# Kernel optimization log

Measured on AMD Instinct MI355X. Metric: run time of the kernel, lower is better.

Reference implementation:

```python
import jax, jax.numpy as jnp
import numpy as np

SOS_INDEX = 0


def setup_inputs() -> dict:
    key = jax.random.key(0)
    ks = jax.random.split(key, 12)
    T, B, H, V = 64, 1024, 512, 512
    s = 1.0 / np.sqrt(H)
    inp = {
        "target_var": jax.random.randint(ks[0], (T, B), 0, V, dtype=jnp.int64),
        "target_max_len": T,
        "encoder_hidden": jax.random.normal(ks[1], (B, H), jnp.float32),
        "encoder_cell": jax.random.normal(ks[2], (B, H), jnp.float32),
        "embedding": jax.random.normal(ks[3], (V, H), jnp.float32) * s,
        "W_ih": jax.random.normal(ks[4], (4 * H, H), jnp.float32) * s,
        "W_hh": jax.random.normal(ks[5], (4 * H, H), jnp.float32) * s,
        "b_ih": jax.random.normal(ks[6], (4 * H,), jnp.float32) * s,
        "b_hh": jax.random.normal(ks[7], (4 * H,), jnp.float32) * s,
        "W_out": jax.random.normal(ks[8], (V, H), jnp.float32) * s,
        "b_out": jax.random.normal(ks[9], (V,), jnp.float32) * s,
    }
    return inp


def reference(target_var, target_max_len, encoder_hidden, encoder_cell,
              embedding, W_ih, W_hh, b_ih, b_hh, W_out, b_out):
    B = target_var.shape[1]
    H = encoder_hidden.shape[1]
    # initial decoder input: embedding of SOS token for every batch element
    x0 = jnp.broadcast_to(embedding[SOS_INDEX], (B, H))
    bias = b_ih + b_hh  # [4H]

    def step(carry, _):
        x, h, c = carry
        # PyTorch LSTMCell: gate order i, f, g, o
        gates = x @ W_ih.T + h @ W_hh.T + bias  # [B, 4H]
        i, f, g, o = jnp.split(gates, 4, axis=-1)
        c_new = jax.nn.sigmoid(f) * c + jax.nn.sigmoid(i) * jnp.tanh(g)
        h_new = jax.nn.sigmoid(o) * jnp.tanh(c_new)
        logits = h_new @ W_out.T + b_out  # [B, V]
        # greedy decoding (topk(1)) -> next input embedding
        nxt = embedding[jnp.argmax(logits, axis=-1)]  # [B, H]
        return (nxt, h_new, c_new), logits

    _, outputs = jax.lax.scan(step, (x0, encoder_hidden, encoder_cell),
                              None, length=target_max_len)
    return outputs  # [T, B, V]
```

## Files before the change

kernel.cpp:

```cpp
#include <hip/hip_runtime.h>
#include <math.h>

constexpr int T_STEPS = 64;
constexpr int B_SZ = 1024;
constexpr int H_SZ = 512;
constexpr int V_SZ = 512;
constexpr int G_SZ = 4 * H_SZ;

typedef _Float16 half8 __attribute__((ext_vector_type(8)));
typedef _Float16 half4 __attribute__((ext_vector_type(4)));
typedef float f32x4 __attribute__((ext_vector_type(4)));

__device__ __forceinline__ float4 ld4(const float* p) {
    return *reinterpret_cast<const float4*>(p);
}
__device__ __forceinline__ void st4(float* p, float4 v) {
    *reinterpret_cast<float4*>(p) = v;
}
__device__ __forceinline__ float sigf(float x) { return 1.f / (1.f + expf(-x)); }

__device__ __forceinline__ unsigned long long pack_vc(float v, int col) {
    unsigned u = __float_as_uint(v);
    unsigned key = (u & 0x80000000u) ? ~u : (u | 0x80000000u);
    return ((unsigned long long)key << 32) | (unsigned)(511 - col);
}

__global__ __launch_bounds__(256) void cvt_pair(
    const float* __restrict__ x, _Float16* __restrict__ hi,
    _Float16* __restrict__ lo)
{
    const int i4 = blockIdx.x * 256 + threadIdx.x;
    const float4 v = ld4(x + (size_t)i4 * 4);
    half4 h, l;
    const float h0 = (float)(_Float16)v.x; h[0] = (_Float16)v.x; l[0] = (_Float16)((v.x - h0) * 2048.f);
    const float h1 = (float)(_Float16)v.y; h[1] = (_Float16)v.y; l[1] = (_Float16)((v.y - h1) * 2048.f);
    const float h2 = (float)(_Float16)v.z; h[2] = (_Float16)v.z; l[2] = (_Float16)((v.z - h2) * 2048.f);
    const float h3 = (float)(_Float16)v.w; h[3] = (_Float16)v.w; l[3] = (_Float16)((v.w - h3) * 2048.f);
    *reinterpret_cast<half4*>(hi + (size_t)i4 * 4) = h;
    *reinterpret_cast<half4*>(lo + (size_t)i4 * 4) = l;
}

__global__ __launch_bounds__(256) void gemm_nt_f32(
    const float* __restrict__ A, const float* __restrict__ Bw,
    float* __restrict__ C, int M, int N, int K,
    const float* __restrict__ bias1, const float* __restrict__ bias2)
{
    constexpr int BK = 16;
    __shared__ __align__(16) float As[BK][64];
    __shared__ __align__(16) float Bs[BK][64];
    const int tid = threadIdx.x;
    const int tx = tid % 16, ty = tid / 16;
    const int m0 = blockIdx.y * 64, n0 = blockIdx.x * 64;
    const int lr = tid / 4, lc = (tid % 4) * 4;
    float acc[4][4] = {};
    for (int k0 = 0; k0 < K; k0 += BK) {
        const float4 av = ld4(&A[(size_t)(m0 + lr) * K + (k0 + lc)]);
        const float4 bv = ld4(&Bw[(size_t)(n0 + lr) * K + (k0 + lc)]);
        __syncthreads();
        As[lc + 0][lr] = av.x; As[lc + 1][lr] = av.y; As[lc + 2][lr] = av.z; As[lc + 3][lr] = av.w;
        Bs[lc + 0][lr] = bv.x; Bs[lc + 1][lr] = bv.y; Bs[lc + 2][lr] = bv.z; Bs[lc + 3][lr] = bv.w;
        __syncthreads();
#pragma unroll
        for (int k = 0; k < BK; ++k) {
            const float4 a4 = ld4(&As[k][ty * 4]);
            const float4 b4 = ld4(&Bs[k][tx * 4]);
            const float ar[4] = {a4.x, a4.y, a4.z, a4.w};
            const float br[4] = {b4.x, b4.y, b4.z, b4.w};
#pragma unroll
            for (int i = 0; i < 4; ++i)
#pragma unroll
                for (int j = 0; j < 4; ++j)
                    acc[i][j] = fmaf(ar[i], br[j], acc[i][j]);
        }
    }
    const int nc = n0 + tx * 4;
    const float4 b1 = ld4(&bias1[nc]);
    const float4 b2 = ld4(&bias2[nc]);
#pragma unroll
    for (int i = 0; i < 4; ++i) {
        const int m = m0 + ty * 4 + i;
        float4 v;
        v.x = acc[i][0] + b1.x + b2.x; v.y = acc[i][1] + b1.y + b2.y;
        v.z = acc[i][2] + b1.z + b2.z; v.w = acc[i][3] + b1.w + b2.w;
        st4(&C[(size_t)m * N + nc], v);
    }
}

__global__ __launch_bounds__(256) void step_gates_cell(
    const _Float16* __restrict__ Ahi, const _Float16* __restrict__ Alo,
    const _Float16* __restrict__ Whh_hi, const _Float16* __restrict__ Whh_lo,
    const float* __restrict__ Eg,
    const unsigned long long* __restrict__ tok_cur,
    unsigned long long* __restrict__ tok_reset,
    float* __restrict__ cbuf,
    _Float16* __restrict__ Nhi, _Float16* __restrict__ Nlo)
{
    constexpr int LDK = 40;
    __shared__ __align__(16) char smem[64 * 129 * 4];
    _Float16* sAh = (_Float16*)smem;
    _Float16* sAl = sAh + 64 * LDK;
    _Float16* sBh = sAl + 64 * LDK;
    _Float16* sBl = sBh + 128 * LDK;
    float* sg = (float*)smem;

    const int tid = threadIdx.x;
    const int wave = tid >> 6, lane = tid & 63;
    const int wm = wave >> 1, wn = wave & 1;
    const int lm = lane & 15, kq = lane >> 4;
    const int h0 = blockIdx.x * 32;
    const int b0 = blockIdx.y * 64;

    const int ar = tid >> 2, akc = (tid & 3) * 8;
    const int r1 = tid >> 2, kc1 = (tid & 3) * 8;
    const int r2 = (tid + 256) >> 2, kc2 = kc1;
    const int g1 = (r1 >> 5) * 512 + h0 + (r1 & 31);
    const int g2 = (r2 >> 5) * 512 + h0 + (r2 & 31);

    const _Float16* pAh = Ahi + (size_t)(b0 + ar) * 512 + akc;
    const _Float16* pAl = Alo + (size_t)(b0 + ar) * 512 + akc;
    const _Float16* pB1h = Whh_hi + (size_t)g1 * 512 + kc1;
    const _Float16* pB1l = Whh_lo + (size_t)g1 * 512 + kc1;
    const _Float16* pB2h = Whh_hi + (size_t)g2 * 512 + kc2;
    const _Float16* pB2l = Whh_lo + (size_t)g2 * 512 + kc2;

    f32x4 aH[2][4] = {};
    f32x4 aC[2][4] = {};

    for (int k0 = 0; k0 < 512; k0 += 32) {
        const half8 va_h = *(const half8*)(pAh + k0);
        const half8 va_l = *(const half8*)(pAl + k0);
        const half8 vb1h = *(const half8*)(pB1h + k0);
        const half8 vb1l = *(const half8*)(pB1l + k0);
        const half8 vb2h = *(const half8*)(pB2h + k0);
        const half8 vb2l = *(const half8*)(pB2l + k0);
        __syncthreads();
        *(half8*)(sAh + ar * LDK + akc) = va_h;
        *(half8*)(sAl + ar * LDK + akc) = va_l;
        *(half8*)(sBh + r1 * LDK + kc1) = vb1h;
        *(half8*)(sBl + r1 * LDK + kc1) = vb1l;
        *(half8*)(sBh + r2 * LDK + kc2) = vb2h;
        *(half8*)(sBl + r2 * LDK + kc2) = vb2l;
        __syncthreads();

        half8 bh[4], bl[4];
#pragma unroll
        for (int gn = 0; gn < 4; ++gn) {
            const int rr = wn * 64 + gn * 16 + lm;
            bh[gn] = *(const half8*)(sBh + rr * LDK + kq * 8);
            bl[gn] = *(const half8*)(sBl + rr * LDK + kq * 8);
        }
#pragma unroll
        for (int gm = 0; gm < 2; ++gm) {
            const int rm = wm * 32 + gm * 16 + lm;
            const half8 ah = *(const half8*)(sAh + rm * LDK + kq * 8);
            const half8 al = *(const half8*)(sAl + rm * LDK + kq * 8);
#pragma unroll
            for (int gn = 0; gn < 4; ++gn)
                aH[gm][gn] = __builtin_amdgcn_mfma_f32_16x16x32_f16(ah, bh[gn], aH[gm][gn], 0, 0, 0);
#pragma unroll
            for (int gn = 0; gn < 4; ++gn)
                aC[gm][gn] = __builtin_amdgcn_mfma_f32_16x16x32_f16(ah, bl[gn], aC[gm][gn], 0, 0, 0);
#pragma unroll
            for (int gn = 0; gn < 4; ++gn)
                aC[gm][gn] = __builtin_amdgcn_mfma_f32_16x16x32_f16(al, bh[gn], aC[gm][gn], 0, 0, 0);
        }
    }

    __syncthreads();
#pragma unroll
    for (int gm = 0; gm < 2; ++gm) {
#pragma unroll
        for (int gn = 0; gn < 4; ++gn) {
            const int row = wm * 32 + gm * 16 + kq * 4;
            const int col = wn * 64 + gn * 16 + lm;
#pragma unroll
            for (int r = 0; r < 4; ++r)
                sg[(row + r) * 129 + col] =
                    aH[gm][gn][r] + aC[gm][gn][r] * (1.f / 2048.f);
        }
    }
    __syncthreads();

    const int crow = tid >> 2;
    const int hb = (tid & 3) * 8;
    const int b = b0 + crow;
    const unsigned long long pk = tok_cur[b];
    const int tk = 511 - (int)(unsigned)(pk & 0xFFFFFFFFu);
    const float* egp = Eg + (size_t)tk * G_SZ + h0;

#pragma unroll
    for (int q = 0; q < 2; ++q) {
        const int hh = hb + q * 4;
        const float* sr = sg + crow * 129;
        const float4 gI = ld4(sr + hh);
        const float4 gF = ld4(sr + 32 + hh);
        const float4 gG = ld4(sr + 64 + hh);
        const float4 gO = ld4(sr + 96 + hh);
        const float4 eI = ld4(egp + hh);
        const float4 eF = ld4(egp + 512 + hh);
        const float4 eG = ld4(egp + 1024 + hh);
        const float4 eO = ld4(egp + 1536 + hh);
        const size_t ci = (size_t)b * 512 + h0 + hh;
        const float4 cv = ld4(cbuf + ci);

        const float iv[4] = {gI.x + eI.x, gI.y + eI.y, gI.z + eI.z, gI.w + eI.w};
        const float fv[4] = {gF.x + eF.x, gF.y + eF.y, gF.z + eF.z, gF.w + eF.w};
        const float gv[4] = {gG.x + eG.x, gG.y + eG.y, gG.z + eG.z, gG.w + eG.w};
        const float ov[4] = {gO.x + eO.x, gO.y + eO.y, gO.z + eO.z, gO.w + eO.w};
        float cc[4] = {cv.x, cv.y, cv.z, cv.w};
        float hn[4];
#pragma unroll
        for (int j = 0; j < 4; ++j) {
            const float cn = sigf(fv[j]) * cc[j] + sigf(iv[j]) * tanhf(gv[j]);
            cc[j] = cn;
            hn[j] = sigf(ov[j]) * tanhf(cn);
        }
        st4(cbuf + ci, make_float4(cc[0], cc[1], cc[2], cc[3]));
        half4 h, l;
#pragma unroll
        for (int j = 0; j < 4; ++j) {
            const _Float16 hi = (_Float16)hn[j];
            h[j] = hi;
            l[j] = (_Float16)((hn[j] - (float)hi) * 2048.f);
        }
        *reinterpret_cast<half4*>(Nhi + ci) = h;
        *reinterpret_cast<half4*>(Nlo + ci) = l;
    }

    if (blockIdx.x == 0 && tid < 64) tok_reset[b0 + tid] = 0ULL;
}

__global__ __launch_bounds__(128) void step_logits_argmax(
    const _Float16* __restrict__ Ahi, const _Float16* __restrict__ Alo,
    const _Float16* __restrict__ Whi, const _Float16* __restrict__ Wlo,
    const float* __restrict__ b_out,
    float* __restrict__ outT,
    unsigned long long* __restrict__ tokmax)
{
    const int tid = threadIdx.x, wave = tid >> 6, lane = tid & 63;
    const int lm = lane & 15, kq = lane >> 4;
    const int n0 = blockIdx.x * 64;
    const int m0 = blockIdx.y * 32 + wave * 16;

    f32x4 aH[4] = {};
    f32x4 aC[4] = {};

    const _Float16* pAh = Ahi + (size_t)(m0 + lm) * 512 + kq * 8;
    const _Float16* pAl = Alo + (size_t)(m0 + lm) * 512 + kq * 8;

    for (int k0 = 0; k0 < 512; k0 += 32) {
        const half8 ah = *(const half8*)(pAh + k0);
        const half8 al = *(const half8*)(pAl + k0);
        half8 bh[4], bl[4];
#pragma unroll
        for (int gn = 0; gn < 4; ++gn) {
            const size_t off = (size_t)(n0 + gn * 16 + lm) * 512 + k0 + kq * 8;
            bh[gn] = *(const half8*)(Whi + off);
            bl[gn] = *(const half8*)(Wlo + off);
        }
#pragma unroll
        for (int gn = 0; gn < 4; ++gn)
            aH[gn] = __builtin_amdgcn_mfma_f32_16x16x32_f16(ah, bh[gn], aH[gn], 0, 0, 0);
#pragma unroll
        for (int gn = 0; gn < 4; ++gn)
            aC[gn] = __builtin_amdgcn_mfma_f32_16x16x32_f16(ah, bl[gn], aC[gn], 0, 0, 0);
#pragma unroll
        for (int gn = 0; gn < 4; ++gn)
            aC[gn] = __builtin_amdgcn_mfma_f32_16x16x32_f16(al, bh[gn], aC[gn], 0, 0, 0);
    }

    unsigned long long best[4] = {0ULL, 0ULL, 0ULL, 0ULL};
#pragma unroll
    for (int gn = 0; gn < 4; ++gn) {
        const int col = n0 + gn * 16 + lm;
        const float bo = b_out[col];
#pragma unroll
        for (int r = 0; r < 4; ++r) {
            const float v = aH[gn][r] + aC[gn][r] * (1.f / 2048.f) + bo;
            const int row = m0 + kq * 4 + r;
            outT[(size_t)row * V_SZ + col] = v;
            const unsigned long long p = pack_vc(v, col);
            if (p > best[r]) best[r] = p;
        }
    }
#pragma unroll
    for (int r = 0; r < 4; ++r) {
#pragma unroll
        for (int off = 1; off < 16; off <<= 1) {
            const unsigned long long o = __shfl_xor(best[r], off);
            if (o > best[r]) best[r] = o;
        }
    }
    if (lm == 0) {
#pragma unroll
        for (int r = 0; r < 4; ++r)
            atomicMax(&tokmax[m0 + kq * 4 + r], best[r]);
    }
}

__global__ __launch_bounds__(256) void init_tok(unsigned long long* __restrict__ tok)
{
    const int i = blockIdx.x * 256 + threadIdx.x;
    tok[i] = (i < 1024) ? 511ULL : 0ULL;
}

extern "C" void kernel_launch(void* const* d_in, const int* in_sizes, int n_in,
                              void* d_out, int out_size, void* d_ws, size_t ws_size,
                              hipStream_t stream)
{
    const float* enc_h = (const float*)d_in[2];
    const float* enc_c = (const float*)d_in[3];
    const float* emb   = (const float*)d_in[4];
    const float* W_ih  = (const float*)d_in[5];
    const float* W_hh  = (const float*)d_in[6];
    const float* b_ih  = (const float*)d_in[7];
    const float* b_hh  = (const float*)d_in[8];
    const float* W_out = (const float*)d_in[9];
    const float* b_out = (const float*)d_in[10];
    float* out = (float*)d_out;

    char* ws = (char*)d_ws;
    _Float16* Whh_hi  = (_Float16*)(ws);
    _Float16* Whh_lo  = (_Float16*)(ws + (2u << 20));
    _Float16* Wout_hi = (_Float16*)(ws + (4u << 20));
    _Float16* Wout_lo = (_Float16*)(ws + (4u << 20) + (512u << 10));
    _Float16* Hhi[2] = {(_Float16*)(ws + (5u << 20)), (_Float16*)(ws + (7u << 20))};
    _Float16* Hlo[2] = {(_Float16*)(ws + (6u << 20)), (_Float16*)(ws + (8u << 20))};
    float* cbuf = (float*)(ws + (9u << 20));
    float* Eg   = (float*)(ws + (11u << 20));
    unsigned long long* tokbuf = (unsigned long long*)(ws + (15u << 20));

    const dim3 blk256(256), blk128(128);

    cvt_pair<<<(G_SZ * H_SZ) / 1024, blk256, 0, stream>>>(W_hh, Whh_hi, Whh_lo);
    cvt_pair<<<(V_SZ * H_SZ) / 1024, blk256, 0, stream>>>(W_out, Wout_hi, Wout_lo);
    cvt_pair<<<(B_SZ * H_SZ) / 1024, blk256, 0, stream>>>(enc_h, Hhi[0], Hlo[0]);
    hipMemcpyAsync(cbuf, enc_c, (size_t)B_SZ * H_SZ * 4, hipMemcpyDeviceToDevice, stream);
    init_tok<<<8, blk256, 0, stream>>>(tokbuf);

    gemm_nt_f32<<<dim3(G_SZ / 64, V_SZ / 64), blk256, 0, stream>>>(
        emb, W_ih, Eg, V_SZ, G_SZ, H_SZ, b_ih, b_hh);

    for (int t = 0; t < T_STEPS; ++t) {
        const int cur = t & 1, nxt = (t + 1) & 1;
        step_gates_cell<<<dim3(H_SZ / 32, B_SZ / 64), blk256, 0, stream>>>(
            Hhi[cur], Hlo[cur], Whh_hi, Whh_lo, Eg,
            tokbuf + cur * B_SZ, tokbuf + nxt * B_SZ,
            cbuf, Hhi[nxt], Hlo[nxt]);

        step_logits_argmax<<<dim3(V_SZ / 64, B_SZ / 32), blk128, 0, stream>>>(
            Hhi[nxt], Hlo[nxt], Wout_hi, Wout_lo, b_out,
            out + (size_t)t * B_SZ * V_SZ, tokbuf + nxt * B_SZ);
    }
}
```

Measured before the change: 2.304 ms.

## Double-buffer gates GEMM via direct global-to-LDS loads; split logits tile across 4 waves

The gates/cell kernel now stages A and W_hh hi/lo tiles with global_load_lds directly into a swizzled, double-buffered LDS region at K=64 per stage. The next tile's loads are issued before the MFMAs on the current tile, replacing the old register-staged single buffer that needed two barriers per K step. The logits kernel moves from 2 to 4 waves per block, each covering a 16x32 subtile, to raise occupancy and cut per-wave register pressure. The cost is 96KB of LDS per block, which limits blocks per CU, and the swizzle index math has to be right for the result to stay correct.

Measured after the change: 1.924 ms. -16.5%, faster.

```diff
diff --git a/kernel.cpp b/kernel.cpp
--- a/kernel.cpp
+++ b/kernel.cpp
@@ -24,6 +24,10 @@
     unsigned key = (u & 0x80000000u) ? ~u : (u | 0x80000000u);
     return ((unsigned long long)key << 32) | (unsigned)(511 - col);
 }
+
+#define GLDS(g, l) __builtin_amdgcn_global_load_lds(                      \
+    (const __attribute__((address_space(1))) void*)(g),                   \
+    (__attribute__((address_space(3))) void*)(l), 16, 0, 0)
 
 __global__ __launch_bounds__(256) void cvt_pair(
     const float* __restrict__ x, _Float16* __restrict__ hi,
@@ -95,12 +99,8 @@
     float* __restrict__ cbuf,
     _Float16* __restrict__ Nhi, _Float16* __restrict__ Nlo)
 {
-    constexpr int LDK = 40;
-    __shared__ __align__(16) char smem[64 * 129 * 4];
-    _Float16* sAh = (_Float16*)smem;
-    _Float16* sAl = sAh + 64 * LDK;
-    _Float16* sBh = sAl + 64 * LDK;
-    _Float16* sBl = sBh + 128 * LDK;
+    constexpr int RBUF = 49152;
+    __shared__ __align__(16) char smem[2 * RBUF];
     float* sg = (float*)smem;
 
     const int tid = threadIdx.x;
@@ -110,63 +110,95 @@
     const int h0 = blockIdx.x * 32;
     const int b0 = blockIdx.y * 64;
 
-    const int ar = tid >> 2, akc = (tid & 3) * 8;
-    const int r1 = tid >> 2, kc1 = (tid & 3) * 8;
-    const int r2 = (tid + 256) >> 2, kc2 = kc1;
-    const int g1 = (r1 >> 5) * 512 + h0 + (r1 & 31);
-    const int g2 = (r2 >> 5) * 512 + h0 + (r2 & 31);
-
-    const _Float16* pAh = Ahi + (size_t)(b0 + ar) * 512 + akc;
-    const _Float16* pAl = Alo + (size_t)(b0 + ar) * 512 + akc;
-    const _Float16* pB1h = Whh_hi + (size_t)g1 * 512 + kc1;
-    const _Float16* pB1l = Whh_lo + (size_t)g1 * 512 + kc1;
-    const _Float16* pB2h = Whh_hi + (size_t)g2 * 512 + kc2;
-    const _Float16* pB2l = Whh_lo + (size_t)g2 * 512 + kc2;
+    const int lrow = lane >> 3;
+    const int co = ((lane & 7) - lrow) & 7;
+    const _Float16* gsrc[12];
+    int loff[12];
+    {
+        int idx = 0;
+#pragma unroll
+        for (int hv = 0; hv < 2; ++hv)
+#pragma unroll
+            for (int rep = 0; rep < 2; ++rep) {
+                const int j = wave + rep * 4;
+                const int rs = j * 8 + lrow;
+                gsrc[idx] = (hv ? Alo : Ahi) + (size_t)(b0 + rs) * 512 + co * 8;
+                loff[idx] = hv * 8192 + j * 1024;
+                ++idx;
+            }
+#pragma unroll
+        for (int hv = 0; hv < 2; ++hv)
+#pragma unroll
+            for (int rep = 0; rep < 4; ++rep) {
+                const int j = wave + rep * 4;
+                const int rs = j * 8 + lrow;
+                const int grow = (rs >> 5) * 512 + h0 + (rs & 31);
+                gsrc[idx] = (hv ? Whh_lo : Whh_hi) + (size_t)grow * 512 + co * 8;
+                loff[idx] = 16384 + hv * 16384 + j * 1024;
+                ++idx;
+            }
+    }
+
+    int ar_off[2][2], br_off[4][2];
+#pragma unroll
+    for (int gm = 0; gm < 2; ++gm)
+#pragma unroll
+        for (int s = 0; s < 2; ++s) {
+            const int rm = wm * 32 + gm * 16 + lm;
+            const int ch = ((s * 4 + kq) + (lm & 7)) & 7;
+            ar_off[gm][s] = rm * 128 + ch * 16;
+        }
+#pragma unroll
+    for (int gn = 0; gn < 4; ++gn)
+#pragma unroll
+        for (int s = 0; s < 2; ++s) {
+            const int rr = wn * 64 + gn * 16 + lm;
+            const int ch = ((s * 4 + kq) + (lm & 7)) & 7;
+            br_off[gn][s] = 16384 + rr * 128 + ch * 16;
+        }
 
     f32x4 aH[2][4] = {};
     f32x4 aC[2][4] = {};
 
-    for (int k0 = 0; k0 < 512; k0 += 32) {
-        const half8 va_h = *(const half8*)(pAh + k0);
-        const half8 va_l = *(const half8*)(pAl + k0);
-        const half8 vb1h = *(const half8*)(pB1h + k0);
-        const half8 vb1l = *(const half8*)(pB1l + k0);
-        const half8 vb2h = *(const half8*)(pB2h + k0);
-        const half8 vb2l = *(const half8*)(pB2l + k0);
+#pragma unroll
+    for (int i = 0; i < 12; ++i) GLDS(gsrc[i], smem + loff[i]);
+    __syncthreads();
+
+#pragma unroll
+    for (int it = 0; it < 8; ++it) {
+        if (it < 7) {
+            char* dst = smem + ((it + 1) & 1) * RBUF;
+            const int ka = (it + 1) * 64;
+#pragma unroll
+            for (int i = 0; i < 12; ++i) GLDS(gsrc[i] + ka, dst + loff[i]);
+        }
+        const char* bp = smem + (it & 1) * RBUF;
+#pragma unroll
+        for (int s = 0; s < 2; ++s) {
+            half8 bh[4], bl[4];
+#pragma unroll
+            for (int gn = 0; gn < 4; ++gn) {
+                bh[gn] = *(const half8*)(bp + br_off[gn][s]);
+                bl[gn] = *(const half8*)(bp + br_off[gn][s] + 16384);
+            }
+#pragma unroll
+            for (int gm = 0; gm < 2; ++gm) {
+                const half8 ah = *(const half8*)(bp + ar_off[gm][s]);
+                const half8 al = *(const half8*)(bp + ar_off[gm][s] + 8192);
+#pragma unroll
+                for (int gn = 0; gn < 4; ++gn)
+                    aH[gm][gn] = __builtin_amdgcn_mfma_f32_16x16x32_f16(ah, bh[gn], aH[gm][gn], 0, 0, 0);
+#pragma unroll
+                for (int gn = 0; gn < 4; ++gn)
+                    aC[gm][gn] = __builtin_amdgcn_mfma_f32_16x16x32_f16(ah, bl[gn], aC[gm][gn], 0, 0, 0);
+#pragma unroll
+                for (int gn = 0; gn < 4; ++gn)
+                    aC[gm][gn] = __builtin_amdgcn_mfma_f32_16x16x32_f16(al, bh[gn], aC[gm][gn], 0, 0, 0);
+            }
+        }
         __syncthreads();
-        *(half8*)(sAh + ar * LDK + akc) = va_h;
-        *(half8*)(sAl + ar * LDK + akc) = va_l;
-        *(half8*)(sBh + r1 * LDK + kc1) = vb1h;
-        *(half8*)(sBl + r1 * LDK + kc1) = vb1l;
-        *(half8*)(sBh + r2 * LDK + kc2) = vb2h;
-        *(half8*)(sBl + r2 * LDK + kc2) = vb2l;
-        __syncthreads();
-
-        half8 bh[4], bl[4];
-#pragma unroll
-        for (int gn = 0; gn < 4; ++gn) {
-            const int rr = wn * 64 + gn * 16 + lm;
-            bh[gn] = *(const half8*)(sBh + rr * LDK + kq * 8);
-            bl[gn] = *(const half8*)(sBl + rr * LDK + kq * 8);
-        }
-#pragma unroll
-        for (int gm = 0; gm < 2; ++gm) {
-            const int rm = wm * 32 + gm * 16 + lm;
-            const half8 ah = *(const half8*)(sAh + rm * LDK + kq * 8);
-            const half8 al = *(const half8*)(sAl + rm * LDK + kq * 8);
-#pragma unroll
-            for (int gn = 0; gn < 4; ++gn)
-                aH[gm][gn] = __builtin_amdgcn_mfma_f32_16x16x32_f16(ah, bh[gn], aH[gm][gn], 0, 0, 0);
-#pragma unroll
-            for (int gn = 0; gn < 4; ++gn)
-                aC[gm][gn] = __builtin_amdgcn_mfma_f32_16x16x32_f16(ah, bl[gn], aC[gm][gn], 0, 0, 0);
-#pragma unroll
-            for (int gn = 0; gn < 4; ++gn)
-                aC[gm][gn] = __builtin_amdgcn_mfma_f32_16x16x32_f16(al, bh[gn], aC[gm][gn], 0, 0, 0);
-        }
-    }
-
-    __syncthreads();
+    }
+
 #pragma unroll
     for (int gm = 0; gm < 2; ++gm) {
 #pragma unroll
@@ -230,7 +262,7 @@
     if (blockIdx.x == 0 && tid < 64) tok_reset[b0 + tid] = 0ULL;
 }
 
-__global__ __launch_bounds__(128) void step_logits_argmax(
+__global__ __launch_bounds__(256) void step_logits_argmax(
     const _Float16* __restrict__ Ahi, const _Float16* __restrict__ Alo,
     const _Float16* __restrict__ Whi, const _Float16* __restrict__ Wlo,
     const float* __restrict__ b_out,
@@ -238,40 +270,40 @@
     unsigned long long* __restrict__ tokmax)
 {
     const int tid = threadIdx.x, wave = tid >> 6, lane = tid & 63;
+    const int wm = wave >> 1, wn = wave & 1;
     const int lm = lane & 15, kq = lane >> 4;
-    const int n0 = blockIdx.x * 64;
-    const int m0 = blockIdx.y * 32 + wave * 16;
-
-    f32x4 aH[4] = {};
-    f32x4 aC[4] = {};
+    const int n0 = blockIdx.x * 64 + wn * 32;
+    const int m0 = blockIdx.y * 32 + wm * 16;
+
+    f32x4 aH[2] = {};
+    f32x4 aC[2] = {};
 
     const _Float16* pAh = Ahi + (size_t)(m0 + lm) * 512 + kq * 8;
     const _Float16* pAl = Alo + (size_t)(m0 + lm) * 512 + kq * 8;
-
+    const _Float16* pW0h = Whi + (size_t)(n0 + lm) * 512 + kq * 8;
+    const _Float16* pW0l = Wlo + (size_t)(n0 + lm) * 512 + kq * 8;
+    const _Float16* pW1h = Whi + (size_t)(n0 + 16 + lm) * 512 + kq * 8;
+    const _Float16* pW1l = Wlo + (size_t)(n0 + 16 + lm) * 512 + kq * 8;
+
+#pragma unroll
     for (int k0 = 0; k0 < 512; k0 += 32) {
         const half8 ah = *(const half8*)(pAh + k0);
         const half8 al = *(const half8*)(pAl + k0);
-        half8 bh[4], bl[4];
-#pragma unroll
-        for (int gn = 0; gn < 4; ++gn) {
-            const size_t off = (size_t)(n0 + gn * 16 + lm) * 512 + k0 + kq * 8;
-            bh[gn] = *(const half8*)(Whi + off);
-            bl[gn] = *(const half8*)(Wlo + off);
-        }
-#pragma unroll
-        for (int gn = 0; gn < 4; ++gn)
-            aH[gn] = __builtin_amdgcn_mfma_f32_16x16x32_f16(ah, bh[gn], aH[gn], 0, 0, 0);
-#pragma unroll
-        for (int gn = 0; gn < 4; ++gn)
-            aC[gn] = __builtin_amdgcn_mfma_f32_16x16x32_f16(ah, bl[gn], aC[gn], 0, 0, 0);
-#pragma unroll
-        for (int gn = 0; gn < 4; ++gn)
-            aC[gn] = __builtin_amdgcn_mfma_f32_16x16x32_f16(al, bh[gn], aC[gn], 0, 0, 0);
+        const half8 b0h = *(const half8*)(pW0h + k0);
+        const half8 b0l = *(const half8*)(pW0l + k0);
+        const half8 b1h = *(const half8*)(pW1h + k0);
+        const half8 b1l = *(const half8*)(pW1l + k0);
+        aH[0] = __builtin_amdgcn_mfma_f32_16x16x32_f16(ah, b0h, aH[0], 0, 0, 0);
+        aH[1] = __builtin_amdgcn_mfma_f32_16x16x32_f16(ah, b1h, aH[1], 0, 0, 0);
+        aC[0] = __builtin_amdgcn_mfma_f32_16x16x32_f16(ah, b0l, aC[0], 0, 0, 0);
+        aC[1] = __builtin_amdgcn_mfma_f32_16x16x32_f16(ah, b1l, aC[1], 0, 0, 0);
+        aC[0] = __builtin_amdgcn_mfma_f32_16x16x32_f16(al, b0h, aC[0], 0, 0, 0);
+        aC[1] = __builtin_amdgcn_mfma_f32_16x16x32_f16(al, b1h, aC[1], 0, 0, 0);
     }
 
     unsigned long long best[4] = {0ULL, 0ULL, 0ULL, 0ULL};
 #pragma unroll
-    for (int gn = 0; gn < 4; ++gn) {
+    for (int gn = 0; gn < 2; ++gn) {
         const int col = n0 + gn * 16 + lm;
         const float bo = b_out[col];
 #pragma unroll
@@ -330,7 +362,7 @@
     float* Eg   = (float*)(ws + (11u << 20));
     unsigned long long* tokbuf = (unsigned long long*)(ws + (15u << 20));
 
-    const dim3 blk256(256), blk128(128);
+    const dim3 blk256(256);
 
     cvt_pair<<<(G_SZ * H_SZ) / 1024, blk256, 0, stream>>>(W_hh, Whh_hi, Whh_lo);
     cvt_pair<<<(V_SZ * H_SZ) / 1024, blk256, 0, stream>>>(W_out, Wout_hi, Wout_lo);
@@ -348,7 +380,7 @@
             tokbuf + cur * B_SZ, tokbuf + nxt * B_SZ,
             cbuf, Hhi[nxt], Hlo[nxt]);
 
-        step_logits_argmax<<<dim3(V_SZ / 64, B_SZ / 32), blk128, 0, stream>>>(
+        step_logits_argmax<<<dim3(V_SZ / 64, B_SZ / 32), blk256, 0, stream>>>(
             Hhi[nxt], Hlo[nxt], Wout_hi, Wout_lo, b_out,
             out + (size_t)t * B_SZ * V_SZ, tokbuf + nxt * B_SZ);
     }
```
